# Optimization experiments

Measured on AMD Instinct MI355X. Metric: run time of the kernel, lower is better.

The kernel has to match this reference:

```python
import jax, jax.numpy as jnp
import numpy as np

B, T, NS, NC, M = 256, 128, 12, 4, 6
MU = 0.1                 # barrier parameter alg.mu
REG_BASE = 1.6           # fp.reg_exp_base
REG = 2.0                # bp.reg
REG_FAC = REG_BASE ** REG - 1.0


def _mt(a):
    return jnp.swapaxes(a, -1, -2)


def setup_inputs():
    key = jax.random.key(0)
    k = jax.random.split(key, 18)
    rn = lambda i, shape: jax.random.normal(k[i], shape, dtype=jnp.float32)
    eye_s = jnp.eye(NS, dtype=jnp.float32)
    eye_c = jnp.eye(NC, dtype=jnp.float32)
    fx = 0.9 * eye_s + 0.02 * rn(0, (B, T, NS, NS))
    fu = 0.1 * rn(1, (B, T, NS, NC))
    fxx = 0.01 * rn(2, (B, T, NS, NS, NS))
    fxu = 0.01 * rn(3, (B, T, NS, NS, NC))
    fuu = 0.01 * rn(4, (B, T, NS, NC, NC))
    qx = 0.1 * rn(5, (B, T, NS))
    qu = 0.1 * rn(6, (B, T, NC))
    Ax = 0.1 * rn(7, (B, T, NS, NS))
    qxx = eye_s + Ax @ _mt(Ax)            # PSD stage cost Hessian
    Au = 0.1 * rn(8, (B, T, NC, NC))
    quu = eye_c + Au @ _mt(Au)            # PD control Hessian
    qxu = 0.05 * rn(9, (B, T, NS, NC))
    cx = 0.1 * rn(10, (B, T, M, NS))
    cu = 0.1 * rn(11, (B, T, M, NC))
    # feasible iterate: c < 0 strictly, dual s > 0
    c = -(jax.random.uniform(k[12], (B, T, M), dtype=jnp.float32) + 0.1)
    s = 0.05 + 0.1 * jax.random.uniform(k[13], (B, T, M), dtype=jnp.float32)
    px = 0.1 * rn(14, (B, NS))
    P = 0.1 * rn(15, (B, NS, NS))
    pxx = eye_s + P @ _mt(P)              # PSD terminal Hessian
    return {"qx": qx, "qu": qu, "qxx": qxx, "qxu": qxu, "quu": quu,
            "fx": fx, "fu": fu, "fxx": fxx, "fxu": fxu, "fuu": fuu,
            "cx": cx, "cu": cu, "c": c, "s": s, "px": px, "pxx": pxx}


def _backward_pass(qx, qu, qxx, qxu, quu, fx, fu, fxx, fxu, fuu, cx, cu, c, s, px, pxx):
    """Feasible-branch ipddp Riccati backward recursion over T steps, batched over B."""
    Bsz = qx.shape[0]

    def step(carry, inp):
        Vx, Vxx, dV0, dV1, qu_err, mu_err = carry
        (qx_t, qu_t, qxx_t, qxu_t, quu_t, fx_t, fu_t,
         fxx_t, fxu_t, fuu_t, cx_t, cu_t, c_t, s_t) = inp
        s_col = s_t[..., None]                      # (B,M,1)
        c_col = c_t[..., None]                      # (B,M,1)
        # Q-function expansions
        Qx = qx_t[..., None] + _mt(cx_t) @ s_col + _mt(fx_t) @ Vx       # (B,NS,1)
        Qu = qu_t[..., None] + _mt(cu_t) @ s_col + _mt(fu_t) @ Vx       # (B,NC,1)
        fxV = _mt(fx_t) @ Vxx
        v = Vx[..., 0]                              # (B,NS)
        Qxx = qxx_t + fxV @ fx_t + jnp.einsum('bs,bsij->bij', v, fxx_t)
        Qxu = qxu_t + fxV @ fu_t + jnp.einsum('bs,bsij->bij', v, fxu_t)
        Quu = quu_t + _mt(fu_t) @ Vxx @ fu_t + jnp.einsum('bs,bsij->bij', v, fuu_t)
        Quu = 0.5 * (Quu + _mt(Quu))
        Quu_reg = Quu + quu_t * REG_FAC
        # interior-point (feasible) modifications
        r = s_col * c_col + MU                      # (B,M,1)
        cinv = 1.0 / c_col
        sc = (s_t / c_t)[..., None]                 # diag(SCinv) entries
        SCcu = sc * cu_t                            # SCinv @ cu
        SCcx = sc * cx_t                            # SCinv @ cx
        cuSCcu = _mt(cu_t) @ SCcu
        Qu = Qu - _mt(cu_t) @ (cinv * r)
        tempQux = _mt(Qxu) - _mt(cu_t) @ SCcx       # (B,NC,NS)
        rhs = jnp.concatenate([Qu, tempQux], axis=-1)   # (B,NC,1+NS)
        kK = -jnp.linalg.solve(Quu_reg - cuSCcu, rhs)
        ku = kK[..., :1]                            # (B,NC,1)
        Ku = kK[..., 1:]                            # (B,NC,NS)
        cuku = cu_t @ ku                            # (B,M,1)
        ks = (-cinv * (r + s_col * cuku))[..., 0]   # (B,M)
        Ks = -(sc * (cx_t + cu_t @ Ku))             # (B,M,NS)
        Quu2 = Quu - cuSCcu
        Qxu2 = _mt(tempQux)
        Qxx2 = Qxx - _mt(cx_t) @ SCcx
        Qx2 = Qx - _mt(cx_t) @ (cinv * r)
        dV0 = dV0 + (_mt(ku) @ Qu)[..., 0, 0]
        dV1 = dV1 + 0.5 * (_mt(ku) @ Quu2 @ ku)[..., 0, 0]
        QxuKu = Qxu2 @ Ku
        KtQ = _mt(Ku) @ Quu2
        Vx_new = Qx2 + _mt(Ku) @ Qu + KtQ @ ku + Qxu2 @ ku
        Vxx_new = Qxx2 + _mt(QxuKu) + QxuKu + KtQ @ Ku
        Vxx_new = 0.5 * (Vxx_new + _mt(Vxx_new))
        qu_err = jnp.maximum(qu_err, jnp.max(jnp.abs(Qu)))
        mu_err = jnp.maximum(mu_err, jnp.max(jnp.abs(r)))
        return (Vx_new, Vxx_new, dV0, dV1, qu_err, mu_err), (ku[..., 0], Ku, ks, Ks)

    xs = tuple(jnp.moveaxis(a, 1, 0) for a in
               (qx, qu, qxx, qxu, quu, fx, fu, fxx, fxu, fuu, cx, cu, c, s))
    zero = jnp.zeros((), jnp.float32)
    init = (px[..., None], pxx, jnp.zeros((Bsz,), jnp.float32),
            jnp.zeros((Bsz,), jnp.float32), zero, zero)
    carry, outs = jax.lax.scan(step, init, xs, reverse=True)
    Vx, Vxx, dV0, dV1, qu_err, mu_err = carry
    ku, Ku, ks, Ks = (jnp.moveaxis(o, 0, 1) for o in outs)
    dV = jnp.stack([dV0, dV1], axis=-1)             # (B,2)
    opterr = jnp.maximum(qu_err, mu_err)            # c_err == 0 in feasible branch
    return ku, Ku, ks, Ks, dV, opterr, Vx[..., 0], Vxx


def reference(qx, qu, qxx, qxu, quu, fx, fu, fxx, fxu, fuu, cx, cu, c, s, px, pxx):
    return _backward_pass(qx, qu, qxx, qxu, quu, fx, fu, fxx, fxu, fuu,
                          cx, cu, c, s, px, pxx)
```

## Files before the change

### kernel.cpp

```cpp
#include <hip/hip_runtime.h>
#include <cstdint>
#include <cstddef>

#define B_  256
#define T_  128
#define NS_ 12
#define NC_ 4
#define M_  6

constexpr float MU_F      = 0.1f;
constexpr float REG_FAC_F = (float)(1.6 * 1.6 - 1.0);

#define OF_FX   0
#define OF_FU   144
#define OF_FXX  192
#define OF_FXU  1920
#define OF_FUU  2496
#define OF_QXX  2688
#define OF_QXU  2832
#define OF_QUU  2880
#define OF_QX   2896
#define OF_QU   2908
#define OF_CX   2912
#define OF_CU   2984
#define OF_C    3008
#define OF_S    3014
#define STG_N   3020

#define O_KU    0
#define O_KUBIG 131072
#define O_KS    1703936
#define O_KSBIG 1900544
#define O_DV    4259840
#define O_OPT   4260352
#define O_VX    4260353
#define O_VXX   4263425

__device__ __forceinline__ void wsync_lds() {
    asm volatile("s_waitcnt lgkmcnt(0)" ::: "memory");
}
__device__ __forceinline__ void wsync_all() {
    asm volatile("s_waitcnt vmcnt(0) lgkmcnt(0)" ::: "memory");
}

__device__ __forceinline__ void gl_lds16(const float* g, float* l) {
    __builtin_amdgcn_global_load_lds((const __attribute__((address_space(1))) void*)g,
                                     (__attribute__((address_space(3))) void*)l, 16, 0, 0);
}
__device__ __forceinline__ void gl_lds4(const float* g, float* l) {
    __builtin_amdgcn_global_load_lds((const __attribute__((address_space(1))) void*)g,
                                     (__attribute__((address_space(3))) void*)l, 4, 0, 0);
}
__device__ __forceinline__ float4 ld4(const float* p)  { return *reinterpret_cast<const float4*>(p); }
__device__ __forceinline__ void   st4(float* p, float4 v) { *reinterpret_cast<float4*>(p) = v; }

__global__ __launch_bounds__(64) void ddp_backward(
    const float* __restrict__ qx,  const float* __restrict__ qu,
    const float* __restrict__ qxx, const float* __restrict__ qxu,
    const float* __restrict__ quu, const float* __restrict__ fx,
    const float* __restrict__ fu,  const float* __restrict__ fxx,
    const float* __restrict__ fxu, const float* __restrict__ fuu,
    const float* __restrict__ cx,  const float* __restrict__ cu,
    const float* __restrict__ c_,  const float* __restrict__ s_,
    const float* __restrict__ px,  const float* __restrict__ pxx,
    float* __restrict__ out, float* __restrict__ ws)
{
    const int l = threadIdx.x;
    const int b = blockIdx.x;

    __shared__ alignas(16) float stg[2][STG_N];
    __shared__ alignas(16) float sVxx[144];
    __shared__ alignas(16) float sVx4[48];
    __shared__ alignas(16) float sG[192];
    __shared__ alignas(16) float sCS[16];
    __shared__ alignas(16) float sSC[8], sCINV[8], sR[8];
    __shared__ alignas(16) float sOUT[192];
    __shared__ alignas(16) float sQuuR[16], sQuu2[16], sM4[16];
    __shared__ alignas(16) float sQP[16];
    __shared__ alignas(16) float sku[4];
    __shared__ alignas(16) float sKu[48];
    __shared__ alignas(16) float sKtQ[48];
    __shared__ float sAcc[4];

    const float* srcs[14] = {qx, qu, qxx, qxu, quu, fx, fu, fxx, fxu, fuu, cx, cu, c_, s_};

    const int up = l & 15, uq = l >> 4;
    const int u_Fo = (up < 12) ? (OF_FX + up) : (OF_FU + up - 12);
    const int u_Fs = (up < 12) ? 12 : 4;
    const int p2    = l - 48;
    const int cs_q0 = (p2 < 12) ? (OF_QX + p2) : (OF_QU + p2 - 12);
    const int cs_cx = (p2 < 12) ? (OF_CX + p2) : (OF_CU + p2 - 12);
    const int cs_cs = (p2 < 12) ? 12 : 4;
    const int cs_Fo = (p2 < 12) ? (OF_FX + p2) : (OF_FU + p2 - 12);
    const int cs_Fs = (p2 < 12) ? 12 : 4;
    const int ai = l >> 2, apq = l & 3;
    const bool a3 = (apq == 3);
    const int a_q0 = a3 ? (OF_QXU + ai*4) : (OF_QXX + ai*12 + apq*4);
    const int a_Fo = a3 ? OF_FU           : (OF_FX + apq*4);
    const int a_Fs = a3 ? 4 : 12;
    const int a_Xo = a3 ? (OF_FXU + ai*4) : (OF_FXX + ai*12 + apq*4);
    const int a_Xs = a3 ? 48 : 144;
    const int a_Co = a3 ? OF_CU           : (OF_CX + apq*4);
    const int a_Cs = a3 ? 4 : 12;
    const int c_cx = (l < 12) ? (OF_CX + l) : (OF_CU + l - 12);
    const int c_cs = (l < 12) ? 12 : 4;
    const int i5 = l / 3, jq5 = l % 3;

    auto prefetch = [&](float* dst, int tt) {
        const uint32_t bt2 = (uint32_t)b * T_ + (uint32_t)tt;
        constexpr int ch_arr[22]  = {5,6,7,7,7,7,7,7,7,8,8,8,9,2,3,4,0,1,10,11,12,13};
        constexpr int ch_goff[22] = {0,0,0,256,512,768,1024,1280,1536,0,256,512,0,0,0,0,0,0,0,0,0,0};
        constexpr int ch_loff[22] = {OF_FX, OF_FU,
                                     OF_FXX, OF_FXX+256, OF_FXX+512, OF_FXX+768,
                                     OF_FXX+1024, OF_FXX+1280, OF_FXX+1536,
                                     OF_FXU, OF_FXU+256, OF_FXU+512,
                                     OF_FUU, OF_QXX, OF_QXU, OF_QUU, OF_QX, OF_QU,
                                     OF_CX, OF_CU, OF_C, OF_S};
        constexpr int ch_nb[22]   = {576,192,1024,1024,1024,1024,1024,1024,768,
                                     1024,1024,256,768,576,192,64,48,16,288,96,24,24};
        constexpr int sl[14]      = {12,4,144,48,16,144,48,1728,576,192,72,24,6,6};
        #pragma unroll
        for (int ci = 0; ci < 22; ++ci) {
            const uint32_t off = bt2 * (uint32_t)sl[ch_arr[ci]] + (uint32_t)ch_goff[ci];
            const float* g = srcs[ch_arr[ci]] + (size_t)off;
            float* dl = dst + ch_loff[ci];
            if ((ch_nb[ci] & 15) == 0) {
                if (l * 16 < ch_nb[ci]) gl_lds16(g + l * 4, dl);
            } else {
                if (l * 4  < ch_nb[ci]) gl_lds4 (g + l,     dl);
            }
        }
    };

    for (int idx = l; idx < 144; idx += 64) sVxx[idx] = pxx[(size_t)b * 144 + idx];
    if (l < 12) st4(sVx4 + l * 4, make_float4(px[(size_t)b * 12 + l], 0.f, 0.f, 0.f));
    prefetch(stg[0], T_ - 1);
    wsync_all();

    float dv0 = 0.f, dv1 = 0.f, qerr = 0.f, merr = 0.f;
    int cur = 0;
    for (int t = T_ - 1; t >= 0; --t) {
        const float* S = stg[cur];
        if (t > 0) prefetch(stg[cur ^ 1], t - 1);
        const uint32_t bt = (uint32_t)b * T_ + (uint32_t)t;

        if (l < 48) {
            const float* F   = S + u_Fo;
            const float* col = sVxx + uq * 4;
            float x0 = 0.f, x1 = 0.f, x2 = 0.f, x3 = 0.f;
            #pragma unroll
            for (int m = 0; m < 12; ++m) {
                const float  f = F[m * u_Fs];
                const float4 v = ld4(col + m * 12);
                x0 += f * v.x; x1 += f * v.y; x2 += f * v.z; x3 += f * v.w;
            }
            st4(sG + up * 12 + uq * 4, make_float4(x0, x1, x2, x3));
        } else {
            float acc = S[cs_q0];
            #pragma unroll
            for (int k = 0; k < 6; ++k)  acc += S[cs_cx + k * cs_cs] * S[OF_S + k];
            #pragma unroll
            for (int m = 0; m < 12; ++m) acc += S[cs_Fo + m * cs_Fs] * sVx4[m * 4];
            sCS[p2] = acc;
        }
        if (l < 6) {
            const float cc = S[OF_C + l], sv = S[OF_S + l];
            sR[l]    = sv * cc + MU_F;
            sCINV[l] = 1.0f / cc;
            sSC[l]   = sv / cc;
        }
        wsync_lds();

        float vx[12], rsc[6], rcinv[6], rr[6];
        #pragma unroll
        for (int s2 = 0; s2 < 12; ++s2) vx[s2] = sVx4[s2 * 4];
        #pragma unroll
        for (int k = 0; k < 6; ++k) { rsc[k] = sSC[k]; rcinv[k] = sCINV[k]; rr[k] = sR[k]; }

        if (l < 48) {
            const float4 g0 = ld4(sG + ai * 12);
            const float4 g1 = ld4(sG + ai * 12 + 4);
            const float4 g2 = ld4(sG + ai * 12 + 8);
            const float gk[12] = {g0.x,g0.y,g0.z,g0.w, g1.x,g1.y,g1.z,g1.w, g2.x,g2.y,g2.z,g2.w};
            float4 acc = ld4(S + a_q0);
            #pragma unroll
            for (int k = 0; k < 12; ++k) {
                const float4 f = ld4(S + a_Fo + k * a_Fs);
                acc.x += gk[k]*f.x; acc.y += gk[k]*f.y; acc.z += gk[k]*f.z; acc.w += gk[k]*f.w;
            }
            #pragma unroll
            for (int s2 = 0; s2 < 12; ++s2) {
                const float4 xv = ld4(S + a_Xo + s2 * a_Xs);
                acc.x += vx[s2]*xv.x; acc.y += vx[s2]*xv.y; acc.z += vx[s2]*xv.z; acc.w += vx[s2]*xv.w;
            }
            #pragma unroll
            for (int k = 0; k < 6; ++k) {
                const float t2 = rsc[k] * S[OF_CX + k * 12 + ai];
                const float4 cv = ld4(S + a_Co + k * a_Cs);
                acc.x -= t2*cv.x; acc.y -= t2*cv.y; acc.z -= t2*cv.z; acc.w -= t2*cv.w;
            }
            st4(sOUT + ai * 16 + apq * 4, acc);
        } else if (l < 52) {
            const int a = l - 48;
            float4 acc = ld4(S + OF_QUU + a * 4);
            #pragma unroll
            for (int k = 0; k < 12; ++k) {
                const float  g = sG[(12 + a) * 12 + k];
                const float4 f = ld4(S + OF_FU + k * 4);
                acc.x += g*f.x; acc.y += g*f.y; acc.z += g*f.z; acc.w += g*f.w;
            }
            #pragma unroll
            for (int s2 = 0; s2 < 12; ++s2) {
                const float4 u = ld4(S + OF_FUU + s2 * 16 + a * 4);
                acc.x += vx[s2]*u.x; acc.y += vx[s2]*u.y; acc.z += vx[s2]*u.z; acc.w += vx[s2]*u.w;
            }
            st4(sQuuR + a * 4, acc);
        }
        if (l < 16) {
            float acc = sCS[l];
            #pragma unroll
            for (int k = 0; k < 6; ++k) acc -= S[c_cx + k * c_cs] * rcinv[k] * rr[k];
            sQP[l] = acc;
        }
        wsync_lds();
        if (l >= 48) {
            const int e = l - 48, ea = e >> 2, eb = e & 3;
            const float q = 0.5f * (sQuuR[e] + sQuuR[eb * 4 + ea]);
            float cs2 = 0.f;
            #pragma unroll
            for (int k = 0; k < 6; ++k) cs2 += rsc[k] * S[OF_CU + k*4 + ea] * S[OF_CU + k*4 + eb];
            const float q2 = q - cs2;
            sQuu2[e] = q2;
            sM4[e]   = q2 + S[OF_QUU + e] * REG_FAC_F;
        }
        wsync_lds();

        if (l < 13) {
            float a00=sM4[0],  a01=sM4[1],  a02=sM4[2],  a03=sM4[3];
            float a10=sM4[4],  a11=sM4[5],  a12=sM4[6],  a13=sM4[7];
            float a20=sM4[8],  a21=sM4[9],  a22=sM4[10], a23=sM4[11];
            float a30=sM4[12], a31=sM4[13], a32=sM4[14], a33=sM4[15];
            const float i0 = 1.0f / a00;
            const float l10 = a10*i0, l20 = a20*i0, l30 = a30*i0;
            a11 -= l10*a01; a12 -= l10*a02; a13 -= l10*a03;
            a21 -= l20*a01; a22 -= l20*a02; a23 -= l20*a03;
            a31 -= l30*a01; a32 -= l30*a02; a33 -= l30*a03;
            const float i1 = 1.0f / a11;
            const float l21 = a21*i1, l31 = a31*i1;
            a22 -= l21*a12; a23 -= l21*a13;
            a32 -= l31*a12; a33 -= l31*a13;
            const float i2 = 1.0f / a22;
            const float l32 = a32*i2;
            a33 -= l32*a23;

            float r0, r1, r2, r3;
            if (l == 0) { const float4 q = ld4(sQP + 12);               r0=q.x; r1=q.y; r2=q.z; r3=q.w; }
            else        { const float4 q = ld4(sOUT + (l-1)*16 + 12);   r0=q.x; r1=q.y; r2=q.z; r3=q.w; }

            const float y0 = r0;
            const float y1 = r1 - l10*y0;
            const float y2 = r2 - l20*y0 - l21*y1;
            const float y3 = r3 - l30*y0 - l31*y1 - l32*y2;
            float x3 = y3 / a33;
            float x2 = (y2 - a23*x3) * i2;
            float x1 = (y1 - a12*x2 - a13*x3) * i1;
            float x0 = (y0 - a01*x1 - a02*x2 - a03*x3) * i0;
            x0 = -x0; x1 = -x1; x2 = -x2; x3 = -x3;

            if (l == 0) {
                sku[0]=x0; sku[1]=x1; sku[2]=x2; sku[3]=x3;
                st4(out + O_KU + (size_t)bt * 4, make_float4(x0, x1, x2, x3));
            } else {
                const int i = l - 1;
                sKu[i]=x0; sKu[12+i]=x1; sKu[24+i]=x2; sKu[36+i]=x3;
                float* Kg = out + O_KUBIG + (size_t)bt * 48;
                Kg[i]=x0; Kg[12+i]=x1; Kg[24+i]=x2; Kg[36+i]=x3;
            }
        } else if (l == 56) {
            float m = 0.f;
            #pragma unroll
            for (int a = 0; a < 4; ++a) m = fmaxf(m, fabsf(sQP[12 + a]));
            qerr = fmaxf(qerr, m);
        } else if (l == 57) {
            float m = 0.f;
            #pragma unroll
            for (int k = 0; k < 6; ++k) m = fmaxf(m, fabsf(rr[k]));
            merr = fmaxf(merr, m);
        }
        wsync_lds();

        if (l < 48) {
            float acc = 0.f;
            #pragma unroll
            for (int b2 = 0; b2 < 4; ++b2) acc += sKu[b2*12 + ai] * sQuu2[b2*4 + apq];
            sKtQ[l] = acc;
        }
        if (l < 18) {
            const int k = i5, iq = jq5;
            const float4 cxv = ld4(S + OF_CX + k*12 + iq*4);
            float a0 = cxv.x, a1 = cxv.y, a2 = cxv.z, a3v = cxv.w;
            #pragma unroll
            for (int a = 0; a < 4; ++a) {
                const float  cua = S[OF_CU + k*4 + a];
                const float4 kv  = ld4(sKu + a*12 + iq*4);
                a0 += cua*kv.x; a1 += cua*kv.y; a2 += cua*kv.z; a3v += cua*kv.w;
            }
            const float ns = -rsc[k];
            st4(out + O_KSBIG + (size_t)bt * 72 + k*12 + iq*4,
                make_float4(ns*a0, ns*a1, ns*a2, ns*a3v));
        } else if (l >= 48 && l < 54) {
            const int k = l - 48;
            float cuku = 0.f;
            #pragma unroll
            for (int a = 0; a < 4; ++a) cuku += S[OF_CU + k*4 + a] * sku[a];
            out[O_KS + (size_t)bt * 6 + k] = -rcinv[k] * (rr[k] + S[OF_S + k] * cuku);
        } else if (l == 54) {
            float d = 0.f;
            #pragma unroll
            for (int a = 0; a < 4; ++a) d += sku[a] * sQP[12 + a];
            dv0 += d;
        } else if (l == 55) {
            float d = 0.f;
            #pragma unroll
            for (int a = 0; a < 4; ++a)
                #pragma unroll
                for (int b2 = 0; b2 < 4; ++b2) d += sku[a] * sQuu2[a*4 + b2] * sku[b2];
            dv1 += 0.5f * d;
        }
        wsync_lds();

        if (l < 36) {
            const int i = i5, jq = jq5;
            const float4 v14  = ld4(sOUT + i*16 + jq*4);
            const float4 tqi4 = ld4(sOUT + i*16 + 12);
            const float4 kqi4 = ld4(sKtQ + i*4);
            const float v1[4]  = {v14.x, v14.y, v14.z, v14.w};
            const float tqi[4] = {tqi4.x, tqi4.y, tqi4.z, tqi4.w};
            const float kqi[4] = {kqi4.x, kqi4.y, kqi4.z, kqi4.w};
            float kuj[4][4], kui[4];
            #pragma unroll
            for (int a = 0; a < 4; ++a) {
                const float4 kv = ld4(sKu + a*12 + jq*4);
                kuj[a][0]=kv.x; kuj[a][1]=kv.y; kuj[a][2]=kv.z; kuj[a][3]=kv.w;
                kui[a] = sKu[a*12 + i];
            }
            float v2[4], tqj[4][4], kqj[4][4];
            #pragma unroll
            for (int r = 0; r < 4; ++r) {
                const int j = jq*4 + r;
                v2[r] = sOUT[j*16 + i];
                const float4 tq = ld4(sOUT + j*16 + 12);
                tqj[r][0]=tq.x; tqj[r][1]=tq.y; tqj[r][2]=tq.z; tqj[r][3]=tq.w;
                const float4 kq = ld4(sKtQ + j*4);
                kqj[r][0]=kq.x; kqj[r][1]=kq.y; kqj[r][2]=kq.z; kqj[r][3]=kq.w;
            }
            float res[4];
            #pragma unroll
            for (int r = 0; r < 4; ++r) {
                float qk = 0.f, kk1 = 0.f, kk2 = 0.f;
                #pragma unroll
                for (int a = 0; a < 4; ++a) {
                    qk  += tqi[a]*kuj[a][r] + tqj[r][a]*kui[a];
                    kk1 += kqi[a]*kuj[a][r];
                    kk2 += kqj[r][a]*kui[a];
                }
                res[r] = 0.5f*(v1[r] + v2[r]) + qk + 0.5f*(kk1 + kk2);
            }
            st4(sVxx + i*12 + jq*4, make_float4(res[0], res[1], res[2], res[3]));
        } else if (l >= 48 && l < 60) {
            const int i = l - 48;
            float acc = sQP[i];
            #pragma unroll
            for (int a = 0; a < 4; ++a)
                acc += sKu[a*12+i]*sQP[12+a] + sKtQ[i*4+a]*sku[a] + sOUT[i*16+12+a]*sku[a];
            st4(sVx4 + i*4, make_float4(acc, 0.f, 0.f, 0.f));
        }
        wsync_all();
        cur ^= 1;
    }

    if (l == 54) sAcc[0] = dv0;
    if (l == 55) sAcc[1] = dv1;
    if (l == 56) sAcc[2] = qerr;
    if (l == 57) sAcc[3] = merr;
    wsync_lds();
    if (l == 0) {
        out[O_DV + b*2 + 0] = sAcc[0];
        out[O_DV + b*2 + 1] = sAcc[1];
        ws[b] = fmaxf(sAcc[2], sAcc[3]);
    }
    if (l < 12) out[O_VX + b*12 + l] = sVx4[l*4];
    for (int idx = l; idx < 144; idx += 64) out[O_VXX + (size_t)b*144 + idx] = sVxx[idx];
}

__global__ __launch_bounds__(256) void opt_reduce(const float* __restrict__ ws,
                                                  float* __restrict__ out)
{
    float v = ws[threadIdx.x];
    #pragma unroll
    for (int o = 32; o > 0; o >>= 1) v = fmaxf(v, __shfl_down(v, o, 64));
    __shared__ float m[4];
    if ((threadIdx.x & 63) == 0) m[threadIdx.x >> 6] = v;
    __syncthreads();
    if (threadIdx.x == 0) out[O_OPT] = fmaxf(fmaxf(m[0], m[1]), fmaxf(m[2], m[3]));
}

extern "C" void kernel_launch(void* const* d_in, const int* in_sizes, int n_in,
                              void* d_out, int out_size, void* d_ws, size_t ws_size,
                              hipStream_t stream) {
    const float* qx  = (const float*)d_in[0];
    const float* qu  = (const float*)d_in[1];
    const float* qxx = (const float*)d_in[2];
    const float* qxu = (const float*)d_in[3];
    const float* quu = (const float*)d_in[4];
    const float* fx  = (const float*)d_in[5];
    const float* fu  = (const float*)d_in[6];
    const float* fxx = (const float*)d_in[7];
    const float* fxu = (const float*)d_in[8];
    const float* fuu = (const float*)d_in[9];
    const float* cx  = (const float*)d_in[10];
    const float* cu  = (const float*)d_in[11];
    const float* c_  = (const float*)d_in[12];
    const float* s_  = (const float*)d_in[13];
    const float* px  = (const float*)d_in[14];
    const float* pxx = (const float*)d_in[15];
    float* out = (float*)d_out;
    float* ws  = (float*)d_ws;

    hipLaunchKernelGGL(ddp_backward, dim3(B_), dim3(64), 0, stream,
                       qx, qu, qxx, qxu, quu, fx, fu, fxx, fxu, fuu,
                       cx, cu, c_, s_, px, pxx, out, ws);
    hipLaunchKernelGGL(opt_reduce, dim3(1), dim3(256), 0, stream, ws, out);
}
```

Measured before the change: 829.6 us.

## Merge Vx into augmented Vxx tile and cut per-step LDS sync phases

Packs Vx as an extra column of a 12x16 LDS tile so the Fᵀ·[Vxx|Vx] product and the constraint-adjusted Qx/Qu gradient are computed in one pass across all 64 lanes. Folds the Quu update into the same wave phase as Qxx/Qxu, and recomputes KᵀQuu2 in registers instead of staging it through LDS. This removes two wave-wide wait points per timestep in the serial recursion. The cost is some redundant arithmetic, and sched_barrier calls that restrict compiler reordering around waits.

```diff
diff --git a/kernel.cpp b/kernel.cpp
--- a/kernel.cpp
+++ b/kernel.cpp
@@ -38,9 +38,11 @@
 
 __device__ __forceinline__ void wsync_lds() {
     asm volatile("s_waitcnt lgkmcnt(0)" ::: "memory");
+    __builtin_amdgcn_sched_barrier(0);
 }
 __device__ __forceinline__ void wsync_all() {
     asm volatile("s_waitcnt vmcnt(0) lgkmcnt(0)" ::: "memory");
+    __builtin_amdgcn_sched_barrier(0);
 }
 
 __device__ __forceinline__ void gl_lds16(const float* g, float* l) {
@@ -69,41 +71,36 @@
     const int b = blockIdx.x;
 
     __shared__ alignas(16) float stg[2][STG_N];
-    __shared__ alignas(16) float sVxx[144];
-    __shared__ alignas(16) float sVx4[48];
+    __shared__ alignas(16) float sVxe[192];
     __shared__ alignas(16) float sG[192];
-    __shared__ alignas(16) float sCS[16];
-    __shared__ alignas(16) float sSC[8], sCINV[8], sR[8];
     __shared__ alignas(16) float sOUT[192];
     __shared__ alignas(16) float sQuuR[16], sQuu2[16], sM4[16];
     __shared__ alignas(16) float sQP[16];
+    __shared__ alignas(16) float sKu[48];
     __shared__ alignas(16) float sku[4];
-    __shared__ alignas(16) float sKu[48];
-    __shared__ alignas(16) float sKtQ[48];
+    __shared__ alignas(16) float sR[8], sCINV[8], sSC[8];
     __shared__ float sAcc[4];
 
     const float* srcs[14] = {qx, qu, qxx, qxu, quu, fx, fu, fxx, fxu, fuu, cx, cu, c_, s_};
 
-    const int up = l & 15, uq = l >> 4;
-    const int u_Fo = (up < 12) ? (OF_FX + up) : (OF_FU + up - 12);
-    const int u_Fs = (up < 12) ? 12 : 4;
-    const int p2    = l - 48;
-    const int cs_q0 = (p2 < 12) ? (OF_QX + p2) : (OF_QU + p2 - 12);
-    const int cs_cx = (p2 < 12) ? (OF_CX + p2) : (OF_CU + p2 - 12);
-    const int cs_cs = (p2 < 12) ? 12 : 4;
-    const int cs_Fo = (p2 < 12) ? (OF_FX + p2) : (OF_FU + p2 - 12);
-    const int cs_Fs = (p2 < 12) ? 12 : 4;
-    const int ai = l >> 2, apq = l & 3;
-    const bool a3 = (apq == 3);
-    const int a_q0 = a3 ? (OF_QXU + ai*4) : (OF_QXX + ai*12 + apq*4);
-    const int a_Fo = a3 ? OF_FU           : (OF_FX + apq*4);
-    const int a_Fs = a3 ? 4 : 12;
-    const int a_Xo = a3 ? (OF_FXU + ai*4) : (OF_FXX + ai*12 + apq*4);
-    const int a_Xs = a3 ? 48 : 144;
-    const int a_Co = a3 ? OF_CU           : (OF_CX + apq*4);
-    const int a_Cs = a3 ? 4 : 12;
-    const int c_cx = (l < 12) ? (OF_CX + l) : (OF_CU + l - 12);
-    const int c_cs = (l < 12) ? 12 : 4;
+    const int p   = l & 15, cq = l >> 4;
+    const bool cq3 = (cq == 3);
+    const int u1_x  = (p < 12) ? (OF_FX + p) : (OF_FU + p - 12);
+    const int u1_xs = (p < 12) ? 12 : 4;
+    const int u1_q0 = (p < 12) ? (OF_QX + p) : (OF_QU + p - 12);
+    const int u1_w  = (p < 12) ? (OF_CX + p) : (OF_CU + p - 12);
+    const int u1_ws = (p < 12) ? 12 : 4;
+    const int pr = l >> 2, q4 = l & 3;
+    const bool q43 = (q4 == 3);
+    const int u2_q0 = (pr < 12) ? (q43 ? (OF_QXU + pr * 4) : (OF_QXX + pr * 12 + q4 * 4))
+                                : (OF_QUU + (pr - 12) * 4);
+    const int u2_x  = q43 ? OF_FU : (OF_FX + q4 * 4);
+    const int u2_xs = q43 ? 4 : 12;
+    const int u2_t  = (pr < 12) ? (q43 ? (OF_FXU + pr * 4) : (OF_FXX + pr * 12 + q4 * 4))
+                                : (OF_FUU + (pr - 12) * 4);
+    const int u2_ts = (pr < 12) ? (q43 ? 48 : 144) : 16;
+    const int u2_w  = q43 ? OF_CU : (OF_CX + q4 * 4);
+    const int u2_ws = q43 ? 4 : 12;
     const int i5 = l / 3, jq5 = l % 3;
 
     auto prefetch = [&](float* dst, int tt) {
@@ -132,8 +129,14 @@
         }
     };
 
-    for (int idx = l; idx < 144; idx += 64) sVxx[idx] = pxx[(size_t)b * 144 + idx];
-    if (l < 12) st4(sVx4 + l * 4, make_float4(px[(size_t)b * 12 + l], 0.f, 0.f, 0.f));
+    #pragma unroll
+    for (int idx = l; idx < 192; idx += 64) {
+        const int r = idx >> 4, ci = idx & 15;
+        float v = 0.f;
+        if (ci < 12)       v = pxx[(size_t)b * 144 + r * 12 + ci];
+        else if (ci == 12) v = px[(size_t)b * 12 + r];
+        sVxe[idx] = v;
+    }
     prefetch(stg[0], T_ - 1);
     wsync_all();
 
@@ -144,94 +147,93 @@
         if (t > 0) prefetch(stg[cur ^ 1], t - 1);
         const uint32_t bt = (uint32_t)b * T_ + (uint32_t)t;
 
-        if (l < 48) {
-            const float* F   = S + u_Fo;
-            const float* col = sVxx + uq * 4;
-            float x0 = 0.f, x1 = 0.f, x2 = 0.f, x3 = 0.f;
+        {
+            if (cq3 && p < 6) {
+                const float cc = S[OF_C + p], sv = S[OF_S + p];
+                sR[p]    = sv * cc + MU_F;
+                sCINV[p] = 1.0f / cc;
+                sSC[p]   = sv / cc;
+            }
+            float accx = 0.f, accy = 0.f, accz = 0.f, accw = 0.f;
+            if (cq3) {
+                float a0 = S[u1_q0];
+                #pragma unroll
+                for (int k = 0; k < 6; ++k) a0 += S[u1_w + k * u1_ws] * S[OF_S + k];
+                accx = a0;
+            }
             #pragma unroll
             for (int m = 0; m < 12; ++m) {
-                const float  f = F[m * u_Fs];
-                const float4 v = ld4(col + m * 12);
-                x0 += f * v.x; x1 += f * v.y; x2 += f * v.z; x3 += f * v.w;
-            }
-            st4(sG + up * 12 + uq * 4, make_float4(x0, x1, x2, x3));
-        } else {
-            float acc = S[cs_q0];
-            #pragma unroll
-            for (int k = 0; k < 6; ++k)  acc += S[cs_cx + k * cs_cs] * S[OF_S + k];
-            #pragma unroll
-            for (int m = 0; m < 12; ++m) acc += S[cs_Fo + m * cs_Fs] * sVx4[m * 4];
-            sCS[p2] = acc;
-        }
-        if (l < 6) {
-            const float cc = S[OF_C + l], sv = S[OF_S + l];
-            sR[l]    = sv * cc + MU_F;
-            sCINV[l] = 1.0f / cc;
-            sSC[l]   = sv / cc;
+                const float  f = S[u1_x + m * u1_xs];
+                const float4 v = ld4(sVxe + m * 16 + cq * 4);
+                accx += f * v.x; accy += f * v.y; accz += f * v.z; accw += f * v.w;
+            }
+            wsync_lds();
+            if (!cq3) {
+                st4(sG + p * 12 + cq * 4, make_float4(accx, accy, accz, accw));
+            } else {
+                #pragma unroll
+                for (int k = 0; k < 6; ++k) accx -= S[u1_w + k * u1_ws] * sCINV[k] * sR[k];
+                sQP[p] = accx;
+            }
         }
         wsync_lds();
 
-        float vx[12], rsc[6], rcinv[6], rr[6];
-        #pragma unroll
-        for (int s2 = 0; s2 < 12; ++s2) vx[s2] = sVx4[s2 * 4];
-        #pragma unroll
-        for (int k = 0; k < 6; ++k) { rsc[k] = sSC[k]; rcinv[k] = sCINV[k]; rr[k] = sR[k]; }
-
-        if (l < 48) {
-            const float4 g0 = ld4(sG + ai * 12);
-            const float4 g1 = ld4(sG + ai * 12 + 4);
-            const float4 g2 = ld4(sG + ai * 12 + 8);
+        {
+            float vx[12];
+            #pragma unroll
+            for (int m = 0; m < 12; ++m) vx[m] = sVxe[m * 16 + 12];
+            float rsc[6];
+            #pragma unroll
+            for (int k = 0; k < 6; ++k) rsc[k] = sSC[k];
+
+            const float4 g0 = ld4(sG + pr * 12);
+            const float4 g1 = ld4(sG + pr * 12 + 4);
+            const float4 g2 = ld4(sG + pr * 12 + 8);
             const float gk[12] = {g0.x,g0.y,g0.z,g0.w, g1.x,g1.y,g1.z,g1.w, g2.x,g2.y,g2.z,g2.w};
-            float4 acc = ld4(S + a_q0);
+
+            float4 acc = ld4(S + u2_q0);
             #pragma unroll
             for (int k = 0; k < 12; ++k) {
-                const float4 f = ld4(S + a_Fo + k * a_Fs);
+                const float4 f = ld4(S + u2_x + k * u2_xs);
                 acc.x += gk[k]*f.x; acc.y += gk[k]*f.y; acc.z += gk[k]*f.z; acc.w += gk[k]*f.w;
             }
             #pragma unroll
             for (int s2 = 0; s2 < 12; ++s2) {
-                const float4 xv = ld4(S + a_Xo + s2 * a_Xs);
-                acc.x += vx[s2]*xv.x; acc.y += vx[s2]*xv.y; acc.z += vx[s2]*xv.z; acc.w += vx[s2]*xv.w;
-            }
-            #pragma unroll
-            for (int k = 0; k < 6; ++k) {
-                const float t2 = rsc[k] * S[OF_CX + k * 12 + ai];
-                const float4 cv = ld4(S + a_Co + k * a_Cs);
-                acc.x -= t2*cv.x; acc.y -= t2*cv.y; acc.z -= t2*cv.z; acc.w -= t2*cv.w;
-            }
-            st4(sOUT + ai * 16 + apq * 4, acc);
-        } else if (l < 52) {
-            const int a = l - 48;
-            float4 acc = ld4(S + OF_QUU + a * 4);
-            #pragma unroll
-            for (int k = 0; k < 12; ++k) {
-                const float  g = sG[(12 + a) * 12 + k];
-                const float4 f = ld4(S + OF_FU + k * 4);
-                acc.x += g*f.x; acc.y += g*f.y; acc.z += g*f.z; acc.w += g*f.w;
-            }
-            #pragma unroll
-            for (int s2 = 0; s2 < 12; ++s2) {
-                const float4 u = ld4(S + OF_FUU + s2 * 16 + a * 4);
-                acc.x += vx[s2]*u.x; acc.y += vx[s2]*u.y; acc.z += vx[s2]*u.z; acc.w += vx[s2]*u.w;
-            }
-            st4(sQuuR + a * 4, acc);
-        }
-        if (l < 16) {
-            float acc = sCS[l];
-            #pragma unroll
-            for (int k = 0; k < 6; ++k) acc -= S[c_cx + k * c_cs] * rcinv[k] * rr[k];
-            sQP[l] = acc;
-        }
-        wsync_lds();
-        if (l >= 48) {
-            const int e = l - 48, ea = e >> 2, eb = e & 3;
-            const float q = 0.5f * (sQuuR[e] + sQuuR[eb * 4 + ea]);
-            float cs2 = 0.f;
-            #pragma unroll
-            for (int k = 0; k < 6; ++k) cs2 += rsc[k] * S[OF_CU + k*4 + ea] * S[OF_CU + k*4 + eb];
-            const float q2 = q - cs2;
-            sQuu2[e] = q2;
-            sM4[e]   = q2 + S[OF_QUU + e] * REG_FAC_F;
+                const float4 tv = ld4(S + u2_t + s2 * u2_ts);
+                acc.x += vx[s2]*tv.x; acc.y += vx[s2]*tv.y; acc.z += vx[s2]*tv.z; acc.w += vx[s2]*tv.w;
+            }
+            if (pr < 12) {
+                #pragma unroll
+                for (int k = 0; k < 6; ++k) {
+                    const float t2 = rsc[k] * S[OF_CX + k * 12 + pr];
+                    const float4 cv = ld4(S + u2_w + k * u2_ws);
+                    acc.x -= t2*cv.x; acc.y -= t2*cv.y; acc.z -= t2*cv.z; acc.w -= t2*cv.w;
+                }
+                st4(sOUT + pr * 16 + q4 * 4, acc);
+            } else if (q43) {
+                st4(sQuuR + (pr - 12) * 4, acc);
+            }
+            wsync_lds();
+            if (pr >= 12 && q43) {
+                const int a = pr - 12;
+                const float accq[4] = {acc.x, acc.y, acc.z, acc.w};
+                float q2v[4];
+                #pragma unroll
+                for (int bb = 0; bb < 4; ++bb) {
+                    const float q = 0.5f * (accq[bb] + sQuuR[bb * 4 + a]);
+                    float cs2 = 0.f;
+                    #pragma unroll
+                    for (int k = 0; k < 6; ++k)
+                        cs2 += rsc[k] * S[OF_CU + k*4 + a] * S[OF_CU + k*4 + bb];
+                    q2v[bb] = q - cs2;
+                }
+                const float4 quuq = ld4(S + OF_QUU + a * 4);
+                st4(sQuu2 + a * 4, make_float4(q2v[0], q2v[1], q2v[2], q2v[3]));
+                st4(sM4   + a * 4, make_float4(q2v[0] + quuq.x * REG_FAC_F,
+                                               q2v[1] + quuq.y * REG_FAC_F,
+                                               q2v[2] + quuq.z * REG_FAC_F,
+                                               q2v[3] + quuq.w * REG_FAC_F));
+            }
         }
         wsync_lds();
 
@@ -254,8 +256,8 @@
             a33 -= l32*a23;
 
             float r0, r1, r2, r3;
-            if (l == 0) { const float4 q = ld4(sQP + 12);               r0=q.x; r1=q.y; r2=q.z; r3=q.w; }
-            else        { const float4 q = ld4(sOUT + (l-1)*16 + 12);   r0=q.x; r1=q.y; r2=q.z; r3=q.w; }
+            if (l == 0) { const float4 q = ld4(sQP + 12);             r0=q.x; r1=q.y; r2=q.z; r3=q.w; }
+            else        { const float4 q = ld4(sOUT + (l-1)*16 + 12); r0=q.x; r1=q.y; r2=q.z; r3=q.w; }
 
             const float y0 = r0;
             const float y1 = r1 - l10*y0;
@@ -270,31 +272,36 @@
             if (l == 0) {
                 sku[0]=x0; sku[1]=x1; sku[2]=x2; sku[3]=x3;
                 st4(out + O_KU + (size_t)bt * 4, make_float4(x0, x1, x2, x3));
+                const float kux[4] = {x0, x1, x2, x3};
+                float d0 = 0.f;
+                #pragma unroll
+                for (int a = 0; a < 4; ++a) d0 += kux[a] * sQP[12 + a];
+                dv0 += d0;
+                float d1 = 0.f;
+                #pragma unroll
+                for (int a = 0; a < 4; ++a)
+                    #pragma unroll
+                    for (int b2 = 0; b2 < 4; ++b2) d1 += kux[a] * sQuu2[a*4 + b2] * kux[b2];
+                dv1 += 0.5f * d1;
             } else {
                 const int i = l - 1;
                 sKu[i]=x0; sKu[12+i]=x1; sKu[24+i]=x2; sKu[36+i]=x3;
                 float* Kg = out + O_KUBIG + (size_t)bt * 48;
                 Kg[i]=x0; Kg[12+i]=x1; Kg[24+i]=x2; Kg[36+i]=x3;
             }
-        } else if (l == 56) {
+        } else if (l == 20) {
             float m = 0.f;
             #pragma unroll
             for (int a = 0; a < 4; ++a) m = fmaxf(m, fabsf(sQP[12 + a]));
             qerr = fmaxf(qerr, m);
-        } else if (l == 57) {
+        } else if (l == 21) {
             float m = 0.f;
             #pragma unroll
-            for (int k = 0; k < 6; ++k) m = fmaxf(m, fabsf(rr[k]));
+            for (int k = 0; k < 6; ++k) m = fmaxf(m, fabsf(sR[k]));
             merr = fmaxf(merr, m);
         }
         wsync_lds();
 
-        if (l < 48) {
-            float acc = 0.f;
-            #pragma unroll
-            for (int b2 = 0; b2 < 4; ++b2) acc += sKu[b2*12 + ai] * sQuu2[b2*4 + apq];
-            sKtQ[l] = acc;
-        }
         if (l < 18) {
             const int k = i5, iq = jq5;
             const float4 cxv = ld4(S + OF_CX + k*12 + iq*4);
@@ -305,38 +312,21 @@
                 const float4 kv  = ld4(sKu + a*12 + iq*4);
                 a0 += cua*kv.x; a1 += cua*kv.y; a2 += cua*kv.z; a3v += cua*kv.w;
             }
-            const float ns = -rsc[k];
+            const float ns = -sSC[k];
             st4(out + O_KSBIG + (size_t)bt * 72 + k*12 + iq*4,
                 make_float4(ns*a0, ns*a1, ns*a2, ns*a3v));
-        } else if (l >= 48 && l < 54) {
-            const int k = l - 48;
-            float cuku = 0.f;
-            #pragma unroll
-            for (int a = 0; a < 4; ++a) cuku += S[OF_CU + k*4 + a] * sku[a];
-            out[O_KS + (size_t)bt * 6 + k] = -rcinv[k] * (rr[k] + S[OF_S + k] * cuku);
-        } else if (l == 54) {
-            float d = 0.f;
-            #pragma unroll
-            for (int a = 0; a < 4; ++a) d += sku[a] * sQP[12 + a];
-            dv0 += d;
-        } else if (l == 55) {
-            float d = 0.f;
-            #pragma unroll
-            for (int a = 0; a < 4; ++a)
-                #pragma unroll
-                for (int b2 = 0; b2 < 4; ++b2) d += sku[a] * sQuu2[a*4 + b2] * sku[b2];
-            dv1 += 0.5f * d;
-        }
-        wsync_lds();
-
+            if (iq == 0) {
+                float cuku = 0.f;
+                #pragma unroll
+                for (int a = 0; a < 4; ++a) cuku += S[OF_CU + k*4 + a] * sku[a];
+                out[O_KS + (size_t)bt * 6 + k] = -sCINV[k] * (sR[k] + S[OF_S + k] * cuku);
+            }
+        }
         if (l < 36) {
             const int i = i5, jq = jq5;
             const float4 v14  = ld4(sOUT + i*16 + jq*4);
             const float4 tqi4 = ld4(sOUT + i*16 + 12);
-            const float4 kqi4 = ld4(sKtQ + i*4);
-            const float v1[4]  = {v14.x, v14.y, v14.z, v14.w};
             const float tqi[4] = {tqi4.x, tqi4.y, tqi4.z, tqi4.w};
-            const float kqi[4] = {kqi4.x, kqi4.y, kqi4.z, kqi4.w};
             float kuj[4][4], kui[4];
             #pragma unroll
             for (int a = 0; a < 4; ++a) {
@@ -344,15 +334,34 @@
                 kuj[a][0]=kv.x; kuj[a][1]=kv.y; kuj[a][2]=kv.z; kuj[a][3]=kv.w;
                 kui[a] = sKu[a*12 + i];
             }
-            float v2[4], tqj[4][4], kqj[4][4];
+            float4 q2r[4];
+            #pragma unroll
+            for (int bb = 0; bb < 4; ++bb) q2r[bb] = ld4(sQuu2 + bb*4);
+            float kqi[4] = {0.f, 0.f, 0.f, 0.f};
+            #pragma unroll
+            for (int bb = 0; bb < 4; ++bb) {
+                kqi[0] += kui[bb]*q2r[bb].x; kqi[1] += kui[bb]*q2r[bb].y;
+                kqi[2] += kui[bb]*q2r[bb].z; kqi[3] += kui[bb]*q2r[bb].w;
+            }
+            float kqj[4][4];
+            #pragma unroll
+            for (int r = 0; r < 4; ++r) { kqj[r][0]=0.f; kqj[r][1]=0.f; kqj[r][2]=0.f; kqj[r][3]=0.f; }
+            #pragma unroll
+            for (int bb = 0; bb < 4; ++bb) {
+                #pragma unroll
+                for (int r = 0; r < 4; ++r) {
+                    kqj[r][0] += kuj[bb][r]*q2r[bb].x; kqj[r][1] += kuj[bb][r]*q2r[bb].y;
+                    kqj[r][2] += kuj[bb][r]*q2r[bb].z; kqj[r][3] += kuj[bb][r]*q2r[bb].w;
+                }
+            }
+            const float v1a[4] = {v14.x, v14.y, v14.z, v14.w};
+            float v2[4], tqj[4][4];
             #pragma unroll
             for (int r = 0; r < 4; ++r) {
                 const int j = jq*4 + r;
                 v2[r] = sOUT[j*16 + i];
                 const float4 tq = ld4(sOUT + j*16 + 12);
                 tqj[r][0]=tq.x; tqj[r][1]=tq.y; tqj[r][2]=tq.z; tqj[r][3]=tq.w;
-                const float4 kq = ld4(sKtQ + j*4);
-                kqj[r][0]=kq.x; kqj[r][1]=kq.y; kqj[r][2]=kq.z; kqj[r][3]=kq.w;
             }
             float res[4];
             #pragma unroll
@@ -364,33 +373,45 @@
                     kk1 += kqi[a]*kuj[a][r];
                     kk2 += kqj[r][a]*kui[a];
                 }
-                res[r] = 0.5f*(v1[r] + v2[r]) + qk + 0.5f*(kk1 + kk2);
-            }
-            st4(sVxx + i*12 + jq*4, make_float4(res[0], res[1], res[2], res[3]));
-        } else if (l >= 48 && l < 60) {
-            const int i = l - 48;
+                res[r] = 0.5f*(v1a[r] + v2[r]) + qk + 0.5f*(kk1 + kk2);
+            }
+            st4(sVxe + i*16 + jq*4, make_float4(res[0], res[1], res[2], res[3]));
+        } else if (l < 48) {
+            const int i = l - 36;
+            float kub[4];
+            #pragma unroll
+            for (int bb = 0; bb < 4; ++bb) kub[bb] = sKu[bb*12 + i];
+            float4 q2r[4];
+            #pragma unroll
+            for (int bb = 0; bb < 4; ++bb) q2r[bb] = ld4(sQuu2 + bb*4);
+            float ktq[4] = {0.f, 0.f, 0.f, 0.f};
+            #pragma unroll
+            for (int bb = 0; bb < 4; ++bb) {
+                ktq[0] += kub[bb]*q2r[bb].x; ktq[1] += kub[bb]*q2r[bb].y;
+                ktq[2] += kub[bb]*q2r[bb].z; ktq[3] += kub[bb]*q2r[bb].w;
+            }
             float acc = sQP[i];
             #pragma unroll
             for (int a = 0; a < 4; ++a)
-                acc += sKu[a*12+i]*sQP[12+a] + sKtQ[i*4+a]*sku[a] + sOUT[i*16+12+a]*sku[a];
-            st4(sVx4 + i*4, make_float4(acc, 0.f, 0.f, 0.f));
+                acc += kub[a]*sQP[12+a] + ktq[a]*sku[a] + sOUT[i*16+12+a]*sku[a];
+            st4(sVxe + i*16 + 12, make_float4(acc, 0.f, 0.f, 0.f));
         }
         wsync_all();
         cur ^= 1;
     }
 
-    if (l == 54) sAcc[0] = dv0;
-    if (l == 55) sAcc[1] = dv1;
-    if (l == 56) sAcc[2] = qerr;
-    if (l == 57) sAcc[3] = merr;
+    if (l == 20) sAcc[2] = qerr;
+    if (l == 21) sAcc[3] = merr;
     wsync_lds();
     if (l == 0) {
-        out[O_DV + b*2 + 0] = sAcc[0];
-        out[O_DV + b*2 + 1] = sAcc[1];
+        out[O_DV + b*2 + 0] = dv0;
+        out[O_DV + b*2 + 1] = dv1;
         ws[b] = fmaxf(sAcc[2], sAcc[3]);
     }
-    if (l < 12) out[O_VX + b*12 + l] = sVx4[l*4];
-    for (int idx = l; idx < 144; idx += 64) out[O_VXX + (size_t)b*144 + idx] = sVxx[idx];
+    if (l < 12) out[O_VX + b*12 + l] = sVxe[l*16 + 12];
+    #pragma unroll
+    for (int idx = l; idx < 144; idx += 64)
+        out[O_VXX + (size_t)b*144 + idx] = sVxe[(idx/12)*16 + (idx%12)];
 }
 
 __global__ __launch_bounds__(256) void opt_reduce(const float* __restrict__ ws,
```

New measurement: 723.8 us. 1.15x faster.
